# Kernel tuning notes

Measured on AMD Instinct MI355X. Metric: run time of the kernel, lower is better.

## Reference

```python
import jax, jax.numpy as jnp
import numpy as np

M, N, D = 100000, 64, 128  # points, channels, voxel grid side


def setup_inputs() -> dict:
    key = jax.random.key(0)
    k1, k2, k3, k4, k5 = jax.random.split(key, 5)
    rng = np.random.default_rng(0)
    # unique occupied voxels in a D^3 grid (Minkowski coords are unique)
    lin = rng.choice(D ** 3, size=M, replace=False)
    coords = np.stack(np.unravel_index(lin, (D, D, D)), axis=1).astype(np.int32)
    w_scale = 0.02  # ~1/sqrt(fan_in=27*N)
    return {
        "feats": jax.random.normal(k1, (M, N), dtype=jnp.float32),
        "W1": jax.random.normal(k2, (27, N, N), dtype=jnp.float32) * w_scale,
        "b1": jax.random.normal(k3, (N,), dtype=jnp.float32) * 0.01,
        "W2": jax.random.normal(k4, (27, N, N), dtype=jnp.float32) * w_scale,
        "b2": jax.random.normal(k5, (N,), dtype=jnp.float32) * 0.01,
        "coords": jnp.asarray(coords),
        "grid_size": D,
    }


def reference(feats, W1, b1, W2, b2, coords, grid_size):
    Dg = grid_size
    m = feats.shape[0]
    # dense hash: linear voxel id -> point index (-1 if empty)
    lin = (coords[:, 0].astype(jnp.int32) * Dg + coords[:, 1]) * Dg + coords[:, 2]
    lookup = jnp.full((Dg * Dg * Dg,), -1, dtype=jnp.int32).at[lin].set(
        jnp.arange(m, dtype=jnp.int32))
    offsets = jnp.array([[i, j, k] for i in (-1, 0, 1) for j in (-1, 0, 1)
                         for k in (-1, 0, 1)], dtype=jnp.int32)  # [27,3]

    def sparse_conv(x, W, b):
        # out[u] = b + sum_k W_k^T gather(x, u+off_k); scan over 27 offsets keeps
        # only one [M,N] gathered buffer live (memory-bound gather-GEMM-scatter)
        def step(acc, wk_off):
            W_k, off = wk_off
            nc = coords + off  # [M,3]
            inb = jnp.all((nc >= 0) & (nc < Dg), axis=1)
            nlin = (nc[:, 0] * Dg + nc[:, 1]) * Dg + nc[:, 2]
            nidx = lookup[jnp.where(inb, nlin, 0)]
            valid = inb & (nidx >= 0)
            g = jnp.where(valid[:, None], x[jnp.maximum(nidx, 0)], 0.0)  # [M,N]
            return acc + g @ W_k, None
        init = jnp.zeros_like(x) + b
        out, _ = jax.lax.scan(step, init, (W, offsets))
        return out

    h = jax.nn.relu(sparse_conv(feats, W1, b1))
    return jax.nn.relu(sparse_conv(h, W2, b2))
```

## Files before the change

kernel.cpp:

```cpp
#include <hip/hip_runtime.h>
#include <hip/hip_bf16.h>
#include <cstdint>
#include <cstddef>

typedef _Float16 half8 __attribute__((ext_vector_type(8)));
typedef float floatx16 __attribute__((ext_vector_type(16)));

#define DGRID 128
#define D3 (DGRID * DGRID * DGRID)
#define WSZ (2 * 27 * 4096)

struct __attribute__((aligned(4))) I3 { int a, b, c; };

__global__ void prep(const int* __restrict__ coords, const float* __restrict__ feats,
                     const float* __restrict__ W1, const float* __restrict__ W2,
                     int* __restrict__ lookup, _Float16* __restrict__ Whf,
                     _Float16* __restrict__ h0, _Float16* __restrict__ h, int M) {
    int tid = blockIdx.x * 256 + threadIdx.x;
    if (tid < WSZ) {
        int idx = tid;
        int j = idx & 7;
        int l = (idx >> 3) & 63;
        int f = (idx >> 9) & 7;
        int kL = idx >> 12;
        int k = kL % 27, L = kL / 27;
        int kk = f & 3, ct = f >> 2;
        int c = kk * 16 + (l >> 5) * 8 + j;
        int n = ct * 32 + (l & 31);
        const float* W = L ? W2 : W1;
        Whf[idx] = (_Float16)W[k * 4096 + c * 64 + n];
        return;
    }
    tid -= WSZ;
    if (tid < M) {
        int x = coords[3 * tid], y = coords[3 * tid + 1], z = coords[3 * tid + 2];
        lookup[(x * DGRID + y) * DGRID + z] = tid;
        return;
    }
    tid -= M;
    if (tid < 64) {
        h0[(size_t)M * 64 + tid] = (_Float16)0.f;
        h[(size_t)M * 64 + tid] = (_Float16)0.f;
        return;
    }
    tid -= 64;
    if (tid < M * 8) {
        const float4* src = (const float4*)feats + (size_t)tid * 2;
        float4 f0 = src[0], f1 = src[1];
        half8 v;
        v[0] = (_Float16)f0.x; v[1] = (_Float16)f0.y;
        v[2] = (_Float16)f0.z; v[3] = (_Float16)f0.w;
        v[4] = (_Float16)f1.x; v[5] = (_Float16)f1.y;
        v[6] = (_Float16)f1.z; v[7] = (_Float16)f1.w;
        ((half8*)h0)[tid] = v;
    }
}

template <bool FIRST, bool OUT_F16>
__global__ __launch_bounds__(64, 2) void spconv(const _Float16* __restrict__ x,
                                                const _Float16* __restrict__ Whf,
                                                const float* __restrict__ bias,
                                                const int* __restrict__ coords,
                                                const int* __restrict__ lookup,
                                                int* __restrict__ nbr,
                                                void* __restrict__ outp, int M) {
    __shared__ int nvs[27 * 64];
    const int lane = threadIdx.x;
    const int lrow = lane & 31;
    const int lhalf = lane >> 5;
    const int mw = blockIdx.x * 64;

    {
        const int row = mw + lane;
        if constexpr (FIRST) {
            if (row < M) {
                int X = coords[3 * row], Y = coords[3 * row + 1], Z = coords[3 * row + 2];
                int zlo = Z - 1;
                if (zlo < 0) zlo = 0;
                if (zlo > DGRID - 3) zlo = DGRID - 3;
                const int zi = Z - zlo;
#pragma unroll
                for (int dx = -1; dx <= 1; ++dx)
#pragma unroll
                    for (int dy = -1; dy <= 1; ++dy) {
                        int nx = X + dx, ny = Y + dy;
                        int v0 = -1, v1 = -1, v2 = -1;
                        if (((unsigned)nx < DGRID) && ((unsigned)ny < DGRID)) {
                            I3 t = *(const I3*)(lookup + ((nx * DGRID + ny) * DGRID + zlo));
                            v0 = t.a; v1 = t.b; v2 = t.c;
                        }
#pragma unroll
                        for (int dz = -1; dz <= 1; ++dz) {
                            int zc = Z + dz;
                            int i = zi + dz;
                            int val = (i == 0) ? v0 : (i == 1) ? v1 : v2;
                            int nidx = M;
                            if (((unsigned)zc < DGRID) && ((unsigned)val < (unsigned)M))
                                nidx = val;
                            int k = (dx + 1) * 9 + (dy + 1) * 3 + (dz + 1);
                            nvs[k * 64 + lane] = nidx;
                            nbr[(size_t)k * M + row] = nidx;
                        }
                    }
            } else {
#pragma unroll
                for (int k = 0; k < 27; ++k) nvs[k * 64 + lane] = M;
            }
        } else {
            const int rc = row < M ? row : M - 1;
#pragma unroll
            for (int k = 0; k < 27; ++k) nvs[k * 64 + lane] = nbr[(size_t)k * M + rc];
        }
    }
    __syncthreads();

    floatx16 acc[4];
#pragma unroll
    for (int i = 0; i < 4; ++i)
#pragma unroll
        for (int j = 0; j < 16; ++j) acc[i][j] = 0.0f;

    const half8* wb = (const half8*)Whf + lane;

    auto loadB = [&](half8* dst, int k) {
#pragma unroll
        for (int f = 0; f < 8; ++f) dst[f] = wb[(k * 8 + f) * 64];
    };
    auto loadA = [&](half8* dst, int n0, int n1) {
        const half8* p0 = (const half8*)(x + (size_t)n0 * 64 + lhalf * 8);
        const half8* p1 = (const half8*)(x + (size_t)n1 * 64 + lhalf * 8);
#pragma unroll
        for (int kk = 0; kk < 4; ++kk) {
            dst[kk] = p0[kk * 2];
            dst[4 + kk] = p1[kk * 2];
        }
    };

    int nv0[4], nv1[4];
#pragma unroll
    for (int j = 0; j < 3; ++j) {
        nv0[j] = nvs[j * 64 + lrow];
        nv1[j] = nvs[j * 64 + 32 + lrow];
    }

    half8 Ar[3][8], Br[2][8];
    loadB(Br[0], 0);
    loadA(Ar[0], nv0[0], nv1[0]);
    loadA(Ar[1], nv0[1], nv1[1]);

#pragma unroll
    for (int i = 0; i < 27; ++i) {
        {
            int jn = i + 3;
            if (jn < 27) {
                nv0[jn & 3] = nvs[jn * 64 + lrow];
                nv1[jn & 3] = nvs[jn * 64 + 32 + lrow];
            }
        }
        if (i + 1 < 27) loadB(Br[(i + 1) & 1], i + 1);
        {
            int ja = i + 2;
            if (ja < 27) loadA(Ar[ja % 3], nv0[ja & 3], nv1[ja & 3]);
        }
        __builtin_amdgcn_sched_barrier(0);
        half8* A = Ar[i % 3];
        half8* B = Br[i & 1];
#pragma unroll
        for (int kk = 0; kk < 4; ++kk)
#pragma unroll
            for (int rt = 0; rt < 2; ++rt)
#pragma unroll
                for (int ct = 0; ct < 2; ++ct)
                    acc[rt * 2 + ct] = __builtin_amdgcn_mfma_f32_32x32x16_f16(
                        A[rt * 4 + kk], B[ct * 4 + kk], acc[rt * 2 + ct], 0, 0, 0);
    }

    const float bv0 = bias[lrow], bv1 = bias[32 + lrow];
#pragma unroll
    for (int rt = 0; rt < 2; ++rt)
#pragma unroll
        for (int ct = 0; ct < 2; ++ct) {
            const float bb = ct ? bv1 : bv0;
#pragma unroll
            for (int reg = 0; reg < 16; ++reg) {
                int row = (reg & 3) + 8 * (reg >> 2) + 4 * lhalf;
                int g = mw + rt * 32 + row;
                if (g < M) {
                    float v = acc[rt * 2 + ct][reg] + bb;
                    v = v > 0.f ? v : 0.f;
                    size_t off = (size_t)g * 64 + ct * 32 + lrow;
                    if constexpr (OUT_F16)
                        ((_Float16*)outp)[off] = (_Float16)v;
                    else
                        ((float*)outp)[off] = v;
                }
            }
        }
}

extern "C" void kernel_launch(void* const* d_in, const int* in_sizes, int n_in,
                              void* d_out, int out_size, void* d_ws, size_t ws_size,
                              hipStream_t stream) {
    const float* feats = (const float*)d_in[0];
    const float* W1 = (const float*)d_in[1];
    const float* b1 = (const float*)d_in[2];
    const float* W2 = (const float*)d_in[3];
    const float* b2 = (const float*)d_in[4];
    const int* coords = (const int*)d_in[5];
    const int M = in_sizes[0] / 64;

    int* lookup = (int*)d_ws;
    int* nbr = lookup + (size_t)D3;
    _Float16* h = (_Float16*)(nbr + (size_t)27 * M);
    _Float16* h0 = h + (size_t)(M + 1) * 64;
    _Float16* Whf = h0 + (size_t)(M + 1) * 64;
    size_t need = (size_t)D3 * 4 + (size_t)27 * M * 4 +
                  2 * (size_t)(M + 1) * 64 * 2 + (size_t)WSZ * 2;
    if (ws_size < need) return;

    long long pt = (long long)WSZ + M + 64 + (long long)M * 8;
    prep<<<(int)((pt + 255) / 256), 256, 0, stream>>>(coords, feats, W1, W2, lookup, Whf,
                                                      h0, h, M);

    int cb = (M + 63) / 64;
    spconv<true, true><<<cb, 64, 0, stream>>>(h0, Whf, b1, coords, lookup, nbr,
                                              (void*)h, M);
    spconv<false, false><<<cb, 64, 0, stream>>>(h, Whf + (size_t)27 * 4096, b2, coords,
                                                lookup, nbr, d_out, M);
}
```

Measured before the change: 171.7 us.

## Process 128 rows per wavefront to amortize weight loads across more MFMAs

Each single-wave block now covers 128 output rows instead of 64. It keeps eight 32x32 accumulator tiles and gathers four row groups per offset, so every weight fragment loaded from global memory feeds twice as many MFMAs. The cost is much higher register pressure: the triple-buffered A set doubles to 48 half8 vectors and the accumulators double as well. The launch bound drops to one wave per SIMD slot and the grid is halved, which reduces occupancy and the latency hiding available for the random row gathers.

```diff
diff --git a/kernel.cpp b/kernel.cpp
--- a/kernel.cpp
+++ b/kernel.cpp
@@ -57,21 +57,23 @@
 }
 
 template <bool FIRST, bool OUT_F16>
-__global__ __launch_bounds__(64, 2) void spconv(const _Float16* __restrict__ x,
+__global__ __launch_bounds__(64, 1) void spconv(const _Float16* __restrict__ x,
                                                 const _Float16* __restrict__ Whf,
                                                 const float* __restrict__ bias,
                                                 const int* __restrict__ coords,
                                                 const int* __restrict__ lookup,
                                                 int* __restrict__ nbr,
                                                 void* __restrict__ outp, int M) {
-    __shared__ int nvs[27 * 64];
+    __shared__ int nvs[27 * 128];
     const int lane = threadIdx.x;
     const int lrow = lane & 31;
     const int lhalf = lane >> 5;
-    const int mw = blockIdx.x * 64;
-
-    {
-        const int row = mw + lane;
+    const int mw = blockIdx.x * 128;
+
+#pragma unroll
+    for (int half = 0; half < 2; ++half) {
+        const int r = half * 64 + lane;
+        const int row = mw + r;
         if constexpr (FIRST) {
             if (row < M) {
                 int X = coords[3 * row], Y = coords[3 * row + 1], Z = coords[3 * row + 2];
@@ -98,25 +100,25 @@
                             if (((unsigned)zc < DGRID) && ((unsigned)val < (unsigned)M))
                                 nidx = val;
                             int k = (dx + 1) * 9 + (dy + 1) * 3 + (dz + 1);
-                            nvs[k * 64 + lane] = nidx;
+                            nvs[k * 128 + r] = nidx;
                             nbr[(size_t)k * M + row] = nidx;
                         }
                     }
             } else {
 #pragma unroll
-                for (int k = 0; k < 27; ++k) nvs[k * 64 + lane] = M;
+                for (int k = 0; k < 27; ++k) nvs[k * 128 + r] = M;
             }
         } else {
             const int rc = row < M ? row : M - 1;
 #pragma unroll
-            for (int k = 0; k < 27; ++k) nvs[k * 64 + lane] = nbr[(size_t)k * M + rc];
+            for (int k = 0; k < 27; ++k) nvs[k * 128 + r] = nbr[(size_t)k * M + rc];
         }
     }
     __syncthreads();
 
-    floatx16 acc[4];
-#pragma unroll
-    for (int i = 0; i < 4; ++i)
+    floatx16 acc[8];
+#pragma unroll
+    for (int i = 0; i < 8; ++i)
 #pragma unroll
         for (int j = 0; j < 16; ++j) acc[i][j] = 0.0f;
 
@@ -126,41 +128,40 @@
 #pragma unroll
         for (int f = 0; f < 8; ++f) dst[f] = wb[(k * 8 + f) * 64];
     };
-    auto loadA = [&](half8* dst, int n0, int n1) {
-        const half8* p0 = (const half8*)(x + (size_t)n0 * 64 + lhalf * 8);
-        const half8* p1 = (const half8*)(x + (size_t)n1 * 64 + lhalf * 8);
-#pragma unroll
-        for (int kk = 0; kk < 4; ++kk) {
-            dst[kk] = p0[kk * 2];
-            dst[4 + kk] = p1[kk * 2];
+    auto loadA = [&](half8* dst, const int* nv) {
+#pragma unroll
+        for (int rt = 0; rt < 4; ++rt) {
+            const half8* p = (const half8*)(x + (size_t)nv[rt] * 64 + lhalf * 8);
+#pragma unroll
+            for (int kk = 0; kk < 4; ++kk) dst[rt * 4 + kk] = p[kk * 2];
         }
     };
 
-    int nv0[4], nv1[4];
-#pragma unroll
-    for (int j = 0; j < 3; ++j) {
-        nv0[j] = nvs[j * 64 + lrow];
-        nv1[j] = nvs[j * 64 + 32 + lrow];
-    }
-
-    half8 Ar[3][8], Br[2][8];
+    int nvr[4][4];
+#pragma unroll
+    for (int j = 0; j < 3; ++j)
+#pragma unroll
+        for (int rt = 0; rt < 4; ++rt) nvr[j][rt] = nvs[j * 128 + rt * 32 + lrow];
+
+    half8 Ar[3][16], Br[2][8];
     loadB(Br[0], 0);
-    loadA(Ar[0], nv0[0], nv1[0]);
-    loadA(Ar[1], nv0[1], nv1[1]);
+    loadA(Ar[0], nvr[0]);
+    loadA(Ar[1], nvr[1]);
 
 #pragma unroll
     for (int i = 0; i < 27; ++i) {
         {
             int jn = i + 3;
             if (jn < 27) {
-                nv0[jn & 3] = nvs[jn * 64 + lrow];
-                nv1[jn & 3] = nvs[jn * 64 + 32 + lrow];
+#pragma unroll
+                for (int rt = 0; rt < 4; ++rt)
+                    nvr[jn & 3][rt] = nvs[jn * 128 + rt * 32 + lrow];
             }
         }
         if (i + 1 < 27) loadB(Br[(i + 1) & 1], i + 1);
         {
             int ja = i + 2;
-            if (ja < 27) loadA(Ar[ja % 3], nv0[ja & 3], nv1[ja & 3]);
+            if (ja < 27) loadA(Ar[ja % 3], nvr[ja & 3]);
         }
         __builtin_amdgcn_sched_barrier(0);
         half8* A = Ar[i % 3];
@@ -168,7 +169,7 @@
 #pragma unroll
         for (int kk = 0; kk < 4; ++kk)
 #pragma unroll
-            for (int rt = 0; rt < 2; ++rt)
+            for (int rt = 0; rt < 4; ++rt)
 #pragma unroll
                 for (int ct = 0; ct < 2; ++ct)
                     acc[rt * 2 + ct] = __builtin_amdgcn_mfma_f32_32x32x16_f16(
@@ -177,7 +178,7 @@
 
     const float bv0 = bias[lrow], bv1 = bias[32 + lrow];
 #pragma unroll
-    for (int rt = 0; rt < 2; ++rt)
+    for (int rt = 0; rt < 4; ++rt)
 #pragma unroll
         for (int ct = 0; ct < 2; ++ct) {
             const float bb = ct ? bv1 : bv0;
@@ -222,7 +223,7 @@
     prep<<<(int)((pt + 255) / 256), 256, 0, stream>>>(coords, feats, W1, W2, lookup, Whf,
                                                       h0, h, M);
 
-    int cb = (M + 63) / 64;
+    int cb = (M + 127) / 128;
     spconv<true, true><<<cb, 64, 0, stream>>>(h0, Whf, b1, coords, lookup, nbr,
                                               (void*)h, M);
     spconv<false, false><<<cb, 64, 0, stream>>>(h, Whf + (size_t)27 * 4096, b2, coords,
```

After: 175.0 us. About the same (+2.0%).

## Reorder points into spatial buckets and swizzle blocks across XCDs for locality

Applied to the files above, without the earlier changes.

Points are counting-sorted into 16^3 spatial buckets (count, scan, scatter kernels), with features and the lookup table written in the sorted order, so that neighbour gathers within a block touch nearby rows. The second conv scatters results back to the original order through the permutation. Block indices are also remapped so that each XCD handles a contiguous range of blocks, which should improve L2 reuse. The cost is four extra small kernel launches plus atomics during preprocessing, and an indirect write on the final output.

```diff
diff --git a/kernel.cpp b/kernel.cpp
--- a/kernel.cpp
+++ b/kernel.cpp
@@ -9,13 +9,14 @@
 #define DGRID 128
 #define D3 (DGRID * DGRID * DGRID)
 #define WSZ (2 * 27 * 4096)
+#define NBUCK 512
 
 struct __attribute__((aligned(4))) I3 { int a, b, c; };
 
-__global__ void prep(const int* __restrict__ coords, const float* __restrict__ feats,
-                     const float* __restrict__ W1, const float* __restrict__ W2,
-                     int* __restrict__ lookup, _Float16* __restrict__ Whf,
-                     _Float16* __restrict__ h0, _Float16* __restrict__ h, int M) {
+
+__global__ void prep0(const float* __restrict__ W1, const float* __restrict__ W2,
+                      _Float16* __restrict__ Whf, int* __restrict__ cnt,
+                      _Float16* __restrict__ h0s, _Float16* __restrict__ h, int M) {
     int tid = blockIdx.x * 256 + threadIdx.x;
     if (tid < WSZ) {
         int idx = tid;
@@ -32,28 +33,65 @@
         return;
     }
     tid -= WSZ;
-    if (tid < M) {
-        int x = coords[3 * tid], y = coords[3 * tid + 1], z = coords[3 * tid + 2];
-        lookup[(x * DGRID + y) * DGRID + z] = tid;
-        return;
-    }
-    tid -= M;
+    if (tid < NBUCK) { cnt[tid] = 0; return; }
+    tid -= NBUCK;
     if (tid < 64) {
-        h0[(size_t)M * 64 + tid] = (_Float16)0.f;
+        h0s[(size_t)M * 64 + tid] = (_Float16)0.f;
         h[(size_t)M * 64 + tid] = (_Float16)0.f;
-        return;
-    }
-    tid -= 64;
-    if (tid < M * 8) {
-        const float4* src = (const float4*)feats + (size_t)tid * 2;
-        float4 f0 = src[0], f1 = src[1];
-        half8 v;
-        v[0] = (_Float16)f0.x; v[1] = (_Float16)f0.y;
-        v[2] = (_Float16)f0.z; v[3] = (_Float16)f0.w;
-        v[4] = (_Float16)f1.x; v[5] = (_Float16)f1.y;
-        v[6] = (_Float16)f1.z; v[7] = (_Float16)f1.w;
-        ((half8*)h0)[tid] = v;
-    }
+    }
+}
+
+__device__ __forceinline__ int bucket_of(int x, int y, int z) {
+    return ((x >> 4) * 8 + (y >> 4)) * 8 + (z >> 4);
+}
+
+__global__ void pcount(const int* __restrict__ coords, int* __restrict__ cnt, int M) {
+    int i = blockIdx.x * 256 + threadIdx.x;
+    if (i >= M) return;
+    int b = bucket_of(coords[3 * i], coords[3 * i + 1], coords[3 * i + 2]);
+    atomicAdd(&cnt[b], 1);
+}
+
+__global__ void pscan(const int* __restrict__ cnt, int* __restrict__ base) {
+    __shared__ int s[NBUCK];
+    int t = threadIdx.x;
+    int my = cnt[t];
+    s[t] = my;
+    __syncthreads();
+    for (int off = 1; off < NBUCK; off <<= 1) {
+        int v = (t >= off) ? s[t - off] : 0;
+        __syncthreads();
+        s[t] += v;
+        __syncthreads();
+    }
+    base[t] = s[t] - my;
+}
+
+__global__ void pscatter(const int* __restrict__ coords, int* __restrict__ base,
+                         int* __restrict__ ord, int* __restrict__ lookup, int M) {
+    int i = blockIdx.x * 256 + threadIdx.x;
+    if (i >= M) return;
+    int x = coords[3 * i], y = coords[3 * i + 1], z = coords[3 * i + 2];
+    int b = bucket_of(x, y, z);
+    int pos = atomicAdd(&base[b], 1);
+    ord[pos] = i;
+    lookup[(x * DGRID + y) * DGRID + z] = pos;
+}
+
+__global__ void pfeat(const float* __restrict__ feats, const int* __restrict__ ord,
+                      _Float16* __restrict__ h0s, int M) {
+    int tid = blockIdx.x * 256 + threadIdx.x;
+    if (tid >= M * 8) return;
+    int s = tid >> 3, j = tid & 7;
+    int i = ord[s];
+    const float4* src = (const float4*)(feats + (size_t)i * 64 + j * 8);
+    float4 f0 = src[0], f1 = src[1];
+    half8 v;
+    v[0] = (_Float16)f0.x; v[1] = (_Float16)f0.y;
+    v[2] = (_Float16)f0.z; v[3] = (_Float16)f0.w;
+    v[4] = (_Float16)f1.x; v[5] = (_Float16)f1.y;
+    v[6] = (_Float16)f1.z; v[7] = (_Float16)f1.w;
+    ((half8*)h0s)[(size_t)s * 8 + j] = v;
 }
 
 template <bool FIRST, bool OUT_F16>
@@ -63,18 +101,24 @@
                                                 const int* __restrict__ coords,
                                                 const int* __restrict__ lookup,
                                                 int* __restrict__ nbr,
+                                                const int* __restrict__ ord,
                                                 void* __restrict__ outp, int M) {
     __shared__ int nvs[27 * 64];
     const int lane = threadIdx.x;
     const int lrow = lane & 31;
     const int lhalf = lane >> 5;
-    const int mw = blockIdx.x * 64;
+    const int nb = gridDim.x;
+    const int xcd = blockIdx.x & 7, loc = blockIdx.x >> 3;
+    const int q = nb >> 3, r = nb & 7;
+    const int swz = (xcd < r ? xcd * (q + 1) : r * (q + 1) + (xcd - r) * q) + loc;
+    const int mw = swz * 64;
 
     {
         const int row = mw + lane;
         if constexpr (FIRST) {
             if (row < M) {
-                int X = coords[3 * row], Y = coords[3 * row + 1], Z = coords[3 * row + 2];
+                const int pi = ord[row];
+                int X = coords[3 * pi], Y = coords[3 * pi + 1], Z = coords[3 * pi + 2];
                 int zlo = Z - 1;
                 if (zlo < 0) zlo = 0;
                 if (zlo > DGRID - 3) zlo = DGRID - 3;
@@ -188,11 +232,12 @@
                 if (g < M) {
                     float v = acc[rt * 2 + ct][reg] + bb;
                     v = v > 0.f ? v : 0.f;
-                    size_t off = (size_t)g * 64 + ct * 32 + lrow;
-                    if constexpr (OUT_F16)
-                        ((_Float16*)outp)[off] = (_Float16)v;
-                    else
-                        ((float*)outp)[off] = v;
+                    if constexpr (OUT_F16) {
+                        ((_Float16*)outp)[(size_t)g * 64 + ct * 32 + lrow] = (_Float16)v;
+                    } else {
+                        int go = ord[g];
+                        ((float*)outp)[(size_t)go * 64 + ct * 32 + lrow] = v;
+                    }
                 }
             }
         }
@@ -212,19 +257,26 @@
     int* lookup = (int*)d_ws;
     int* nbr = lookup + (size_t)D3;
     _Float16* h = (_Float16*)(nbr + (size_t)27 * M);
-    _Float16* h0 = h + (size_t)(M + 1) * 64;
-    _Float16* Whf = h0 + (size_t)(M + 1) * 64;
+    _Float16* h0s = h + (size_t)(M + 1) * 64;
+    _Float16* Whf = h0s + (size_t)(M + 1) * 64;
+    int* cnt = (int*)(Whf + (size_t)WSZ);
+    int* base = cnt + NBUCK;
+    int* ord = base + NBUCK;
     size_t need = (size_t)D3 * 4 + (size_t)27 * M * 4 +
-                  2 * (size_t)(M + 1) * 64 * 2 + (size_t)WSZ * 2;
+                  2 * (size_t)(M + 1) * 64 * 2 + (size_t)WSZ * 2 +
+                  (size_t)(2 * NBUCK + M) * 4;
     if (ws_size < need) return;
 
-    long long pt = (long long)WSZ + M + 64 + (long long)M * 8;
-    prep<<<(int)((pt + 255) / 256), 256, 0, stream>>>(coords, feats, W1, W2, lookup, Whf,
-                                                      h0, h, M);
+    long long p0t = (long long)WSZ + NBUCK + 64;
+    prep0<<<(int)((p0t + 255) / 256), 256, 0, stream>>>(W1, W2, Whf, cnt, h0s, h, M);
+    pcount<<<(M + 255) / 256, 256, 0, stream>>>(coords, cnt, M);
+    pscan<<<1, NBUCK, 0, stream>>>(cnt, base);
+    pscatter<<<(M + 255) / 256, 256, 0, stream>>>(coords, base, ord, lookup, M);
+    pfeat<<<(M * 8 + 255) / 256, 256, 0, stream>>>(feats, ord, h0s, M);
 
     int cb = (M + 63) / 64;
-    spconv<true, true><<<cb, 64, 0, stream>>>(h0, Whf, b1, coords, lookup, nbr,
+    spconv<true, true><<<cb, 64, 0, stream>>>(h0s, Whf, b1, coords, lookup, nbr, ord,
                                               (void*)h, M);
     spconv<false, false><<<cb, 64, 0, stream>>>(h, Whf + (size_t)27 * 4096, b2, coords,
-                                                lookup, nbr, d_out, M);
-}
+                                                lookup, nbr, ord, d_out, M);
+}
```

Result: slower. 238.7 us (+39.1%).

## Stage gathered neighbor rows into LDS via direct global-to-LDS loads

Applied to the files above, without the earlier changes.

The gathered A-operand rows now go through double-buffered, XOR-swizzled shared memory filled with global_load_lds, instead of being loaded straight into registers from scattered rows. Each row is fetched as contiguous 128-byte segments by eight lanes, which gives better coalescing, and register pressure drops from holding three A buffers. The cost is manual vmcnt waits with a hardcoded count, plus a prefetch depth of one offset instead of two. There is no barrier on the LDS buffer reuse, which relies on a single-wave block.

```diff
diff --git a/kernel.cpp b/kernel.cpp
--- a/kernel.cpp
+++ b/kernel.cpp
@@ -65,9 +65,12 @@
                                                 int* __restrict__ nbr,
                                                 void* __restrict__ outp, int M) {
     __shared__ int nvs[27 * 64];
+    __shared__ _Float16 abuf[2][4096];
     const int lane = threadIdx.x;
     const int lrow = lane & 31;
     const int lhalf = lane >> 5;
+    const int r8 = lane >> 3;
+    const int c8 = lane & 7;
     const int mw = blockIdx.x * 64;
 
     {
@@ -126,53 +129,58 @@
 #pragma unroll
         for (int f = 0; f < 8; ++f) dst[f] = wb[(k * 8 + f) * 64];
     };
-    auto loadA = [&](half8* dst, int n0, int n1) {
-        const half8* p0 = (const half8*)(x + (size_t)n0 * 64 + lhalf * 8);
-        const half8* p1 = (const half8*)(x + (size_t)n1 * 64 + lhalf * 8);
+
+    auto stageA = [&](int buf, int k) {
+#pragma unroll
+        for (int s = 0; s < 8; ++s) {
+            int nv = nvs[k * 64 + s * 8 + r8];
+            const _Float16* src = x + (size_t)nv * 64 + (c8 ^ r8) * 8;
+            __builtin_amdgcn_global_load_lds(
+                (const __attribute__((address_space(1))) void*)src,
+                (__attribute__((address_space(3))) void*)&abuf[buf][s * 512],
+                16, 0, 0);
+        }
+    };
+
+    auto readA = [&](half8* dst, int buf, int rt) {
+        const _Float16* base = &abuf[buf][(rt * 32 + lrow) * 64];
+        const int key = lrow & 7;
 #pragma unroll
         for (int kk = 0; kk < 4; ++kk) {
-            dst[kk] = p0[kk * 2];
-            dst[4 + kk] = p1[kk * 2];
+            int slot = (lhalf + kk * 2) ^ key;
+            dst[kk] = *(const half8*)(base + slot * 8);
         }
     };
 
-    int nv0[4], nv1[4];
-#pragma unroll
-    for (int j = 0; j < 3; ++j) {
-        nv0[j] = nvs[j * 64 + lrow];
-        nv1[j] = nvs[j * 64 + 32 + lrow];
-    }
-
-    half8 Ar[3][8], Br[2][8];
+    half8 Br[2][8];
+    stageA(0, 0);
     loadB(Br[0], 0);
-    loadA(Ar[0], nv0[0], nv1[0]);
-    loadA(Ar[1], nv0[1], nv1[1]);
 
 #pragma unroll
     for (int i = 0; i < 27; ++i) {
-        {
-            int jn = i + 3;
-            if (jn < 27) {
-                nv0[jn & 3] = nvs[jn * 64 + lrow];
-                nv1[jn & 3] = nvs[jn * 64 + 32 + lrow];
+        if (i + 1 < 27) {
+            stageA((i + 1) & 1, i + 1);
+            loadB(Br[(i + 1) & 1], i + 1);
+        }
+        __builtin_amdgcn_sched_barrier(0);
+        if (i + 1 < 27)
+            asm volatile("s_waitcnt vmcnt(16)" ::: "memory");
+        else
+            asm volatile("s_waitcnt vmcnt(0)" ::: "memory");
+        __builtin_amdgcn_sched_barrier(0);
+        half8 a0[4], a1[4];
+        readA(a0, i & 1, 0);
+        readA(a1, i & 1, 1);
+        half8* B = Br[i & 1];
+#pragma unroll
+        for (int kk = 0; kk < 4; ++kk)
+#pragma unroll
+            for (int ct = 0; ct < 2; ++ct) {
+                acc[0 * 2 + ct] = __builtin_amdgcn_mfma_f32_32x32x16_f16(
+                    a0[kk], B[ct * 4 + kk], acc[0 * 2 + ct], 0, 0, 0);
+                acc[1 * 2 + ct] = __builtin_amdgcn_mfma_f32_32x32x16_f16(
+                    a1[kk], B[ct * 4 + kk], acc[1 * 2 + ct], 0, 0, 0);
             }
-        }
-        if (i + 1 < 27) loadB(Br[(i + 1) & 1], i + 1);
-        {
-            int ja = i + 2;
-            if (ja < 27) loadA(Ar[ja % 3], nv0[ja & 3], nv1[ja & 3]);
-        }
-        __builtin_amdgcn_sched_barrier(0);
-        half8* A = Ar[i % 3];
-        half8* B = Br[i & 1];
-#pragma unroll
-        for (int kk = 0; kk < 4; ++kk)
-#pragma unroll
-            for (int rt = 0; rt < 2; ++rt)
-#pragma unroll
-                for (int ct = 0; ct < 2; ++ct)
-                    acc[rt * 2 + ct] = __builtin_amdgcn_mfma_f32_32x32x16_f16(
-                        A[rt * 4 + kk], B[ct * 4 + kk], acc[rt * 2 + ct], 0, 0, 0);
     }
 
     const float bv0 = bias[lrow], bv1 = bias[32 + lrow];
```

New measurement: 200.3 us. 16.7% more time.
